# Performance work log

Hardware: AMD Instinct MI355X
Metric: run time of the kernel (lower is better)

## Reference

```python
import jax, jax.numpy as jnp
import numpy as np

D_MODEL = 1024
N_HEADS = 16


def setup_inputs() -> dict:
    key = jax.random.key(0)
    ks = jax.random.split(key, 11)
    B, S = 4, 2048
    sc = 1.0 / np.sqrt(D_MODEL)
    inp = {
        "Q": jax.random.normal(ks[0], (B, S, D_MODEL), jnp.float32),
        "K": jax.random.normal(ks[1], (B, S, D_MODEL), jnp.float32),
        "V": jax.random.normal(ks[2], (B, S, D_MODEL), jnp.float32),
        "Wq": jax.random.normal(ks[3], (D_MODEL, D_MODEL), jnp.float32) * sc,
        "bq": jnp.zeros((D_MODEL,), jnp.float32),
        "Wk": jax.random.normal(ks[4], (D_MODEL, D_MODEL), jnp.float32) * sc,
        "bk": jnp.zeros((D_MODEL,), jnp.float32),
        "Wv": jax.random.normal(ks[5], (D_MODEL, D_MODEL), jnp.float32) * sc,
        "bv": jnp.zeros((D_MODEL,), jnp.float32),
        "Wo": jax.random.normal(ks[6], (D_MODEL, D_MODEL), jnp.float32) * sc,
        "bo": jnp.zeros((D_MODEL,), jnp.float32),
    }
    return inp


def reference(Q, K, V, Wq, bq, Wk, bk, Wv, bv, Wo, bo):
    B, Sq, d_model = Q.shape
    h = N_HEADS
    d_k = d_model // h

    def split_heads(x, W, b):
        y = x @ W.T + b                     # (B, S, d_model)
        return y.reshape(B, x.shape[1], h, d_k).transpose(0, 2, 1, 3)  # (B,h,S,d_k)

    q = split_heads(Q, Wq, bq)
    k = split_heads(K, Wk, bk)
    v = split_heads(V, Wv, bv)

    scores = jnp.einsum("bhqd,bhkd->bhqk", q, k) / jnp.sqrt(jnp.asarray(d_k, q.dtype))
    attn = jax.nn.softmax(scores.astype(jnp.float32), axis=-1).astype(q.dtype)
    out = jnp.einsum("bhqk,bhkd->bhqd", attn, v)  # (B,h,Sq,d_k)
    out = out.transpose(0, 2, 1, 3).reshape(B, Sq, d_model)
    return out @ Wo.T + bo
```

## Files before the change

kernel.cpp:

```cpp
#include <hip/hip_runtime.h>
#include <stdint.h>

#define DM    1024
#define NH    16
#define DKH   64
#define SEQ   2048
#define NB    4
#define MROWS (NB * SEQ)

typedef __attribute__((ext_vector_type(4))) float f32x4;
typedef __attribute__((ext_vector_type(8))) short s16x8;
typedef __attribute__((ext_vector_type(4))) unsigned short u16x4;
typedef __attribute__((ext_vector_type(8))) unsigned short u16x8;

__device__ __forceinline__ unsigned short f2bf(float f) {
  union { float f; uint32_t u; } v; v.f = f;
  uint32_t r = v.u + 0x7fffu + ((v.u >> 16) & 1u);
  return (unsigned short)(r >> 16);
}

__device__ __forceinline__ void gload16(const void* g, void* l) {
  __builtin_amdgcn_global_load_lds(
      (__attribute__((address_space(1))) void*)(uintptr_t)g,
      (__attribute__((address_space(3))) void*)(uint32_t)(uintptr_t)l,
      16, 0, 0);
}

__device__ __forceinline__ float exp2fast(float x) {
#if __has_builtin(__builtin_amdgcn_exp2f)
  return __builtin_amdgcn_exp2f(x);
#else
  return exp2f(x);
#endif
}

__device__ __forceinline__ unsigned int cvtpk(float a, float b) {
  unsigned int r;
  asm("v_cvt_pk_bf16_f32 %0, %1, %2" : "=v"(r) : "v"(a), "v"(b));
  return r;
}

__device__ __forceinline__ float bperm(float v, int srclane) {
  union { float f; int i; } u; u.f = v;
  u.i = __builtin_amdgcn_ds_bpermute(srclane << 2, u.i);
  return u.f;
}

__device__ __forceinline__ void cvt8(const float* in, unsigned short* out, int i) {
  const f32x4* p = (const f32x4*)(in + i);
  f32x4 a = p[0], b = p[1];
  u16x8 r;
#pragma unroll
  for (int j = 0; j < 4; ++j) { r[j] = f2bf(a[j]); r[4 + j] = f2bf(b[j]); }
  *(u16x8*)(out + i) = r;
}

__global__ __launch_bounds__(256) void cvt4_kernel(const float* __restrict__ a,
                                                   const float* __restrict__ b,
                                                   const float* __restrict__ c,
                                                   const float* __restrict__ d,
                                                   unsigned short* __restrict__ oa,
                                                   unsigned short* __restrict__ ob,
                                                   unsigned short* __restrict__ oc,
                                                   unsigned short* __restrict__ od) {
  const int seg = blockIdx.x >> 9;
  const int blk = blockIdx.x & 511;
  const float* in = (seg == 0) ? a : (seg == 1) ? b : (seg == 2) ? c : d;
  unsigned short* out = (seg == 0) ? oa : (seg == 1) ? ob : (seg == 2) ? oc : od;
  cvt8(in, out, (blk * 256 + threadIdx.x) * 8);
}

template <int MODE, int AFP32>
__global__ __launch_bounds__(256) void gemm_bt(const void* __restrict__ Ap,
                                               const unsigned short* __restrict__ Bw,
                                               const float* __restrict__ bias,
                                               void* __restrict__ out,
                                               float oscale) {
  __shared__ char smem[65536];

  int bid = (int)(blockIdx.y * 8 + blockIdx.x);
  bid = (bid & 7) * 64 + (bid >> 3);
  const int tcol = (bid & 7) * 128;
  const int trow = (bid >> 3) * 128;

  const int lane = threadIdx.x & 63;
  const int w    = threadIdx.x >> 6;
  const int wm = w >> 1, wn = w & 1;
  const int l15 = lane & 15, l4 = lane >> 4;

  const float* Af = (const float*)Ap;
  const unsigned short* Ah = (const unsigned short*)Ap;

  const int srow = w * 8 + (lane >> 3);
  const int sc   = ((lane & 7) ^ (lane >> 3)) * 8;
  const int ldst = (lane & 7) * 16;

  f32x4 acc[4][4] = {};
  f32x4 areg[4][2];

  auto aload = [&](int k0) {
#pragma unroll
    for (int i = 0; i < 4; ++i) {
      const float* p = Af + (size_t)(trow + i * 32 + srow) * DM + k0 + sc;
      areg[i][0] = *(const f32x4*)p;
      areg[i][1] = *(const f32x4*)(p + 4);
    }
  };
  auto awrite = [&](int buf) {
    char* As = smem + buf * 32768;
#pragma unroll
    for (int i = 0; i < 4; ++i) {
      union { unsigned int u[4]; s16x8 v; } pu;
      pu.u[0] = cvtpk(areg[i][0][0], areg[i][0][1]);
      pu.u[1] = cvtpk(areg[i][0][2], areg[i][0][3]);
      pu.u[2] = cvtpk(areg[i][1][0], areg[i][1][1]);
      pu.u[3] = cvtpk(areg[i][1][2], areg[i][1][3]);
      *(s16x8*)(As + (i * 32 + srow) * 128 + ldst) = pu.v;
    }
  };
  auto astage = [&](int buf, int k0) {
    char* As = smem + buf * 32768;
#pragma unroll
    for (int i = 0; i < 4; ++i)
      gload16(Ah + (size_t)(trow + i * 32 + srow) * DM + k0 + sc, As + i * 4096 + w * 1024);
  };
  auto bstage = [&](int buf, int k0) {
    char* Bs = smem + buf * 32768 + 16384;
#pragma unroll
    for (int i = 0; i < 4; ++i)
      gload16(Bw + (size_t)(tcol + i * 32 + srow) * DM + k0 + sc, Bs + i * 4096 + w * 1024);
  };
  auto compute = [&](int buf) {
    char* As = smem + buf * 32768;
    char* Bs = As + 16384;
#pragma unroll
    for (int ks = 0; ks < 2; ++ks) {
      s16x8 af[4], bf[4];
#pragma unroll
      for (int x = 0; x < 4; ++x) {
        const int ra = wm * 64 + x * 16 + l15;
        const int rb = wn * 64 + x * 16 + l15;
        const int kb = ks * 4 + l4;
        af[x] = *(const s16x8*)(As + ra * 128 + ((kb ^ (ra & 7)) << 4));
        bf[x] = *(const s16x8*)(Bs + rb * 128 + ((kb ^ (rb & 7)) << 4));
      }
#pragma unroll
      for (int mi = 0; mi < 4; ++mi)
#pragma unroll
        for (int ni = 0; ni < 4; ++ni)
          acc[mi][ni] = __builtin_amdgcn_mfma_f32_16x16x32_bf16(af[mi], bf[ni], acc[mi][ni], 0, 0, 0);
    }
  };

  if (AFP32) aload(0); else astage(0, 0);
  bstage(0, 0);
  if (AFP32) awrite(0);
  __syncthreads();
  int cur = 0;

  for (int k0 = 0; k0 < DM; k0 += 64) {
    const bool more = (k0 + 64 < DM);
    if (more) {
      if (AFP32) aload(k0 + 64); else astage(cur ^ 1, k0 + 64);
      bstage(cur ^ 1, k0 + 64);
    }
    compute(cur);
    if (more && AFP32) awrite(cur ^ 1);
    __syncthreads();
    cur ^= 1;
  }

#pragma unroll
  for (int ni = 0; ni < 4; ++ni) {
    const int n  = tcol + wn * 64 + ni * 16 + l15;
    const float bv = bias[n];
#pragma unroll
    for (int mi = 0; mi < 4; ++mi) {
      const int m0 = trow + wm * 64 + mi * 16 + l4 * 4;
      if (MODE == 2) {
        float* o = (float*)out;
#pragma unroll
        for (int j = 0; j < 4; ++j)
          o[(size_t)(m0 + j) * DM + n] = acc[mi][ni][j] + bv;
      } else if (MODE == 0) {
        unsigned short* o = (unsigned short*)out;
        const int bb = m0 >> 11, h = n >> 6, dk = n & 63;
#pragma unroll
        for (int j = 0; j < 4; ++j) {
          const int s = (m0 + j) & 2047;
          o[(((size_t)bb * NH + h) * SEQ + s) * DKH + dk] = f2bf((acc[mi][ni][j] + bv) * oscale);
        }
      } else {
        unsigned short* o = (unsigned short*)out;
        const int bb = m0 >> 11, h = n >> 6, dk = n & 63, s = m0 & 2047;
        const int u = s & 31;
        const int s2 = (s & ~31) | ((u & 12) << 1) | ((u & 16) >> 2);
        u16x4 pk;
#pragma unroll
        for (int j = 0; j < 4; ++j) pk[j] = f2bf(acc[mi][ni][j] + bv);
        *(u16x4*)(o + (((size_t)bb * NH + h) * DKH + dk) * SEQ + s2) = pk;
      }
    }
  }
}

__global__ __launch_bounds__(256, 2) void attn_kernel(const unsigned short* __restrict__ qh,
                                                      const unsigned short* __restrict__ kh,
                                                      const unsigned short* __restrict__ vth,
                                                      unsigned short* __restrict__ ao) {
  __shared__ char smem[32768];

  int bid = (int)blockIdx.x;
  bid = (bid & 7) * 64 + (bid >> 3);
  const int bh = bid >> 3;
  const int q0 = (bid & 7) * 256;

  const int lane = threadIdx.x & 63;
  const int w    = threadIdx.x >> 6;
  const int l15 = lane & 15, l4 = lane >> 4;

  const int qrow = q0 + w * 64;
  const unsigned short* qbase = qh + ((size_t)bh * SEQ + qrow) * DKH;

  s16x8 qf[4][2];
#pragma unroll
  for (int ni = 0; ni < 4; ++ni)
#pragma unroll
    for (int ks = 0; ks < 2; ++ks)
      qf[ni][ks] = *(const s16x8*)(qbase + (ni * 16 + l15) * DKH + ks * 32 + l4 * 8);

  int koff[2][4], voff[2][4];
#pragma unroll
  for (int ks = 0; ks < 2; ++ks)
#pragma unroll
    for (int mi = 0; mi < 4; ++mi) {
      const int r = mi * 16 + l15;
      koff[ks][mi] = r * 128 + (((ks * 4 + l4) ^ (r & 7)) << 4);
    }
#pragma unroll
  for (int m = 0; m < 2; ++m)
#pragma unroll
    for (int nd = 0; nd < 4; ++nd) {
      const int r = nd * 16 + l15;
      voff[m][nd] = r * 128 + (((m * 4 + l4) ^ (r & 7)) << 4);
    }

  f32x4 o[4][4] = {};
  f32x4 lsum[4] = {};

  s16x8 onesB = (s16x8)0;
  if (l15 == 0) {
#pragma unroll
    for (int j = 0; j < 8; ++j) onesB[j] = (short)0x3F80;
  }

  const unsigned short* kbase = kh  + (size_t)bh * SEQ * DKH;
  const unsigned short* vbase = vth + (size_t)bh * DKH * SEQ;

  auto stageK = [&](int buf, int kv0) {
    char* Ks = smem + buf * 8192;
#pragma unroll
    for (int i = 0; i < 2; ++i) {
      const int row = i * 32 + w * 8 + (lane >> 3);
      const int sc  = ((lane & 7) ^ (row & 7)) << 3;
      gload16(kbase + (size_t)(kv0 + row) * DKH + sc, Ks + i * 4096 + w * 1024);
    }
  };
  auto stageV = [&](int buf, int kv0) {
    char* Vs = smem + 16384 + buf * 8192;
#pragma unroll
    for (int i = 0; i < 2; ++i) {
      const int row = i * 32 + w * 8 + (lane >> 3);
      const int sc  = ((lane & 7) ^ (row & 7)) << 3;
      gload16(vbase + (size_t)row * SEQ + kv0 + sc, Vs + i * 4096 + w * 1024);
    }
  };

  f32x4 sa[4][4];

  auto qkt = [&](const char* Ks) {
#pragma unroll
    for (int mi = 0; mi < 4; ++mi)
#pragma unroll
      for (int ni = 0; ni < 4; ++ni) sa[mi][ni] = (f32x4)0.f;
    __builtin_amdgcn_s_setprio(1);
#pragma unroll
    for (int ks = 0; ks < 2; ++ks) {
      s16x8 kf[4];
#pragma unroll
      for (int mi = 0; mi < 4; ++mi) kf[mi] = *(const s16x8*)(Ks + koff[ks][mi]);
#pragma unroll
      for (int mi = 0; mi < 4; ++mi)
#pragma unroll
        for (int ni = 0; ni < 4; ++ni)
          sa[mi][ni] = __builtin_amdgcn_mfma_f32_16x16x32_bf16(kf[mi], qf[ni][ks], sa[mi][ni], 0, 0, 0);
    }
    __builtin_amdgcn_s_setprio(0);
  };

  auto smpv = [&](const char* Vs) {
#pragma unroll
    for (int mi = 0; mi < 4; ++mi)
#pragma unroll
      for (int ni = 0; ni < 4; ++ni)
#pragma unroll
        for (int j = 0; j < 4; ++j)
          sa[mi][ni][j] = exp2fast(sa[mi][ni][j]);

    __builtin_amdgcn_s_setprio(1);
#pragma unroll
    for (int m = 0; m < 2; ++m) {
      s16x8 pa[4];
#pragma unroll
      for (int ni = 0; ni < 4; ++ni) {
        union { unsigned int u[4]; s16x8 v; } pu;
        pu.u[0] = cvtpk(sa[2 * m][ni][0],     sa[2 * m][ni][1]);
        pu.u[1] = cvtpk(sa[2 * m][ni][2],     sa[2 * m][ni][3]);
        pu.u[2] = cvtpk(sa[2 * m + 1][ni][0], sa[2 * m + 1][ni][1]);
        pu.u[3] = cvtpk(sa[2 * m + 1][ni][2], sa[2 * m + 1][ni][3]);
        pa[ni] = pu.v;
      }
#pragma unroll
      for (int ni = 0; ni < 4; ++ni)
        lsum[ni] = __builtin_amdgcn_mfma_f32_16x16x32_bf16(pa[ni], onesB, lsum[ni], 0, 0, 0);
#pragma unroll
      for (int nd = 0; nd < 4; ++nd) {
        const s16x8 vbf = *(const s16x8*)(Vs + voff[m][nd]);
#pragma unroll
        for (int ni = 0; ni < 4; ++ni)
          o[ni][nd] = __builtin_amdgcn_mfma_f32_16x16x32_bf16(pa[ni], vbf, o[ni][nd], 0, 0, 0);
      }
    }
    __builtin_amdgcn_s_setprio(0);
  };

  stageK(0, 0); stageV(0, 0);
  __syncthreads();

  for (int t = 0; t < 32; t += 2) {
    const int kv0 = t * 64;
    stageK(1, kv0 + 64); stageV(1, kv0 + 64);
    qkt(smem);
    smpv(smem + 16384);
    __syncthreads();
    if (t + 2 < 32) { stageK(0, kv0 + 128); stageV(0, kv0 + 128); }
    qkt(smem + 8192);
    smpv(smem + 16384 + 8192);
    __syncthreads();
  }

  const int bb = bh >> 4, h = bh & 15;
#pragma unroll
  for (int ni = 0; ni < 4; ++ni) {
#pragma unroll
    for (int j = 0; j < 4; ++j) {
      const float inv = 1.0f / bperm(lsum[ni][j], lane & 48);
      const int s = qrow + ni * 16 + l4 * 4 + j;
#pragma unroll
      for (int nd = 0; nd < 4; ++nd) {
        const int col = h * 64 + nd * 16 + l15;
        ao[((size_t)bb * SEQ + s) * DM + col] = f2bf(o[ni][nd][j] * inv);
      }
    }
  }
}

extern "C" void kernel_launch(void* const* d_in, const int* in_sizes, int n_in,
                              void* d_out, int out_size, void* d_ws, size_t ws_size,
                              hipStream_t stream) {
  const float* Q  = (const float*)d_in[0];
  const float* K  = (const float*)d_in[1];
  const float* V  = (const float*)d_in[2];
  const float* Wq = (const float*)d_in[3];
  const float* bq = (const float*)d_in[4];
  const float* Wk = (const float*)d_in[5];
  const float* bk = (const float*)d_in[6];
  const float* Wv = (const float*)d_in[7];
  const float* bv = (const float*)d_in[8];
  const float* Wo = (const float*)d_in[9];
  const float* bo = (const float*)d_in[10];
  float* out = (float*)d_out;

  char* ws = (char*)d_ws;
  const size_t MB = 1024 * 1024;
  unsigned short* Wqb = (unsigned short*)(ws + 0 * MB);
  unsigned short* Wkb = (unsigned short*)(ws + 2 * MB);
  unsigned short* Wvb = (unsigned short*)(ws + 4 * MB);
  unsigned short* Wob = (unsigned short*)(ws + 6 * MB);
  unsigned short* qhd = (unsigned short*)(ws + 8 * MB);
  unsigned short* khd = (unsigned short*)(ws + 24 * MB);
  unsigned short* vtd = (unsigned short*)(ws + 40 * MB);
  unsigned short* aod = (unsigned short*)(ws + 56 * MB);

  const float QSCALE = 0.18033688011112042f;

  cvt4_kernel<<<dim3(4 * 512), 256, 0, stream>>>(Wq, Wk, Wv, Wo, Wqb, Wkb, Wvb, Wob);

  dim3 gg(DM / 128, MROWS / 128);
  gemm_bt<0, 1><<<gg, 256, 0, stream>>>(Q, Wqb, bq, qhd, QSCALE);
  gemm_bt<0, 1><<<gg, 256, 0, stream>>>(K, Wkb, bk, khd, 1.0f);
  gemm_bt<1, 1><<<gg, 256, 0, stream>>>(V, Wvb, bv, vtd, 1.0f);

  attn_kernel<<<dim3(512), 256, 0, stream>>>(qhd, khd, vtd, aod);

  gemm_bt<2, 0><<<gg, 256, 0, stream>>>(aod, Wob, bo, out, 1.0f);
}
```

Baseline: 164.4 us.

## Merge QKV projections into one launch and use fine-grained waitcnt barriers

The three QKV projection GEMMs become a single launch, with blockIdx.z choosing the input, weight and output layout. This removes two launch gaps and gives more blocks in flight at once. In the GEMMs and the attention loop, full __syncthreads is replaced by explicit vmcnt/lgkmcnt waits plus s_barrier, so the next tile's loads can stay in flight while the current tile computes, and setprio is raised around the MFMA sections. The cost is that correctness now rests on hand-counted outstanding-load numbers. Also, the gemm_out loop drops the barrier after the last iteration and relies on the counts being right.

```diff
diff --git a/kernel.cpp b/kernel.cpp
--- a/kernel.cpp
+++ b/kernel.cpp
@@ -45,6 +45,11 @@
   u.i = __builtin_amdgcn_ds_bpermute(srclane << 2, u.i);
   return u.f;
 }
+
+#define WAIT_VM(N)  do { asm volatile("s_waitcnt vmcnt(" #N ")" ::: "memory"); \
+                         __builtin_amdgcn_sched_barrier(0); } while (0)
+#define WAIT_LGKM0  do { asm volatile("s_waitcnt lgkmcnt(0)" ::: "memory"); \
+                         __builtin_amdgcn_sched_barrier(0); } while (0)
 
 __device__ __forceinline__ void cvt8(const float* in, unsigned short* out, int i) {
   const f32x4* p = (const f32x4*)(in + i);
@@ -70,13 +75,28 @@
   cvt8(in, out, (blk * 256 + threadIdx.x) * 8);
 }
 
-template <int MODE, int AFP32>
-__global__ __launch_bounds__(256) void gemm_bt(const void* __restrict__ Ap,
-                                               const unsigned short* __restrict__ Bw,
-                                               const float* __restrict__ bias,
-                                               void* __restrict__ out,
-                                               float oscale) {
+__global__ __launch_bounds__(256) void gemm_qkv(const float* __restrict__ Aq,
+                                                const float* __restrict__ Ak,
+                                                const float* __restrict__ Av,
+                                                const unsigned short* __restrict__ Wq,
+                                                const unsigned short* __restrict__ Wk,
+                                                const unsigned short* __restrict__ Wv,
+                                                const float* __restrict__ biq,
+                                                const float* __restrict__ bik,
+                                                const float* __restrict__ biv,
+                                                unsigned short* __restrict__ oq,
+                                                unsigned short* __restrict__ ok,
+                                                unsigned short* __restrict__ ov,
+                                                float qscale) {
   __shared__ char smem[65536];
+
+  const int z = blockIdx.z;
+  const float* Af = (z == 0) ? Aq : (z == 1) ? Ak : Av;
+  const unsigned short* Bw = (z == 0) ? Wq : (z == 1) ? Wk : Wv;
+  const float* bias = (z == 0) ? biq : (z == 1) ? bik : biv;
+  unsigned short* out = (z == 0) ? oq : (z == 1) ? ok : ov;
+  const float oscale = (z == 0) ? qscale : 1.0f;
+  const int mode = (z == 2) ? 1 : 0;
 
   int bid = (int)(blockIdx.y * 8 + blockIdx.x);
   bid = (bid & 7) * 64 + (bid >> 3);
@@ -87,9 +107,6 @@
   const int w    = threadIdx.x >> 6;
   const int wm = w >> 1, wn = w & 1;
   const int l15 = lane & 15, l4 = lane >> 4;
-
-  const float* Af = (const float*)Ap;
-  const unsigned short* Ah = (const unsigned short*)Ap;
 
   const int srow = w * 8 + (lane >> 3);
   const int sc   = ((lane & 7) ^ (lane >> 3)) * 8;
@@ -118,12 +135,6 @@
       *(s16x8*)(As + (i * 32 + srow) * 128 + ldst) = pu.v;
     }
   };
-  auto astage = [&](int buf, int k0) {
-    char* As = smem + buf * 32768;
-#pragma unroll
-    for (int i = 0; i < 4; ++i)
-      gload16(Ah + (size_t)(trow + i * 32 + srow) * DM + k0 + sc, As + i * 4096 + w * 1024);
-  };
   auto bstage = [&](int buf, int k0) {
     char* Bs = smem + buf * 32768 + 16384;
 #pragma unroll
@@ -133,6 +144,7 @@
   auto compute = [&](int buf) {
     char* As = smem + buf * 32768;
     char* Bs = As + 16384;
+    __builtin_amdgcn_s_setprio(1);
 #pragma unroll
     for (int ks = 0; ks < 2; ++ks) {
       s16x8 af[4], bf[4];
@@ -150,23 +162,32 @@
         for (int ni = 0; ni < 4; ++ni)
           acc[mi][ni] = __builtin_amdgcn_mfma_f32_16x16x32_bf16(af[mi], bf[ni], acc[mi][ni], 0, 0, 0);
     }
-  };
-
-  if (AFP32) aload(0); else astage(0, 0);
+    __builtin_amdgcn_s_setprio(0);
+  };
+
+  aload(0);
   bstage(0, 0);
-  if (AFP32) awrite(0);
-  __syncthreads();
+  awrite(0);
+  WAIT_VM(0);
+  WAIT_LGKM0;
+  __builtin_amdgcn_s_barrier();
   int cur = 0;
 
   for (int k0 = 0; k0 < DM; k0 += 64) {
     const bool more = (k0 + 64 < DM);
     if (more) {
-      if (AFP32) aload(k0 + 64); else astage(cur ^ 1, k0 + 64);
+      aload(k0 + 64);
       bstage(cur ^ 1, k0 + 64);
+      WAIT_VM(12);
+    } else {
+      WAIT_VM(0);
     }
     compute(cur);
-    if (more && AFP32) awrite(cur ^ 1);
-    __syncthreads();
+    if (more) {
+      awrite(cur ^ 1);
+      WAIT_LGKM0;
+      __builtin_amdgcn_s_barrier();
+    }
     cur ^= 1;
   }
 
@@ -177,29 +198,108 @@
 #pragma unroll
     for (int mi = 0; mi < 4; ++mi) {
       const int m0 = trow + wm * 64 + mi * 16 + l4 * 4;
-      if (MODE == 2) {
-        float* o = (float*)out;
-#pragma unroll
-        for (int j = 0; j < 4; ++j)
-          o[(size_t)(m0 + j) * DM + n] = acc[mi][ni][j] + bv;
-      } else if (MODE == 0) {
-        unsigned short* o = (unsigned short*)out;
-        const int bb = m0 >> 11, h = n >> 6, dk = n & 63;
+      const int bb = m0 >> 11, h = n >> 6, dk = n & 63;
+      if (mode == 0) {
 #pragma unroll
         for (int j = 0; j < 4; ++j) {
           const int s = (m0 + j) & 2047;
-          o[(((size_t)bb * NH + h) * SEQ + s) * DKH + dk] = f2bf((acc[mi][ni][j] + bv) * oscale);
+          out[(((size_t)bb * NH + h) * SEQ + s) * DKH + dk] = f2bf((acc[mi][ni][j] + bv) * oscale);
         }
       } else {
-        unsigned short* o = (unsigned short*)out;
-        const int bb = m0 >> 11, h = n >> 6, dk = n & 63, s = m0 & 2047;
+        const int s = m0 & 2047;
         const int u = s & 31;
         const int s2 = (s & ~31) | ((u & 12) << 1) | ((u & 16) >> 2);
         u16x4 pk;
 #pragma unroll
         for (int j = 0; j < 4; ++j) pk[j] = f2bf(acc[mi][ni][j] + bv);
-        *(u16x4*)(o + (((size_t)bb * NH + h) * DKH + dk) * SEQ + s2) = pk;
+        *(u16x4*)(out + (((size_t)bb * NH + h) * DKH + dk) * SEQ + s2) = pk;
       }
+    }
+  }
+}
+
+__global__ __launch_bounds__(256) void gemm_out(const unsigned short* __restrict__ Ah,
+                                                const unsigned short* __restrict__ Bw,
+                                                const float* __restrict__ bias,
+                                                float* __restrict__ out) {
+  __shared__ char smem[65536];
+
+  int bid = (int)(blockIdx.y * 8 + blockIdx.x);
+  bid = (bid & 7) * 64 + (bid >> 3);
+  const int tcol = (bid & 7) * 128;
+  const int trow = (bid >> 3) * 128;
+
+  const int lane = threadIdx.x & 63;
+  const int w    = threadIdx.x >> 6;
+  const int wm = w >> 1, wn = w & 1;
+  const int l15 = lane & 15, l4 = lane >> 4;
+
+  const int srow = w * 8 + (lane >> 3);
+  const int sc   = ((lane & 7) ^ (lane >> 3)) * 8;
+
+  f32x4 acc[4][4] = {};
+
+  auto stage = [&](int buf, int k0) {
+    char* As = smem + buf * 32768;
+    char* Bs = As + 16384;
+#pragma unroll
+    for (int i = 0; i < 4; ++i) {
+      gload16(Ah + (size_t)(trow + i * 32 + srow) * DM + k0 + sc, As + i * 4096 + w * 1024);
+      gload16(Bw + (size_t)(tcol + i * 32 + srow) * DM + k0 + sc, Bs + i * 4096 + w * 1024);
+    }
+  };
+  auto compute = [&](int buf) {
+    char* As = smem + buf * 32768;
+    char* Bs = As + 16384;
+    __builtin_amdgcn_s_setprio(1);
+#pragma unroll
+    for (int ks = 0; ks < 2; ++ks) {
+      s16x8 af[4], bf[4];
+#pragma unroll
+      for (int x = 0; x < 4; ++x) {
+        const int ra = wm * 64 + x * 16 + l15;
+        const int rb = wn * 64 + x * 16 + l15;
+        const int kb = ks * 4 + l4;
+        af[x] = *(const s16x8*)(As + ra * 128 + ((kb ^ (ra & 7)) << 4));
+        bf[x] = *(const s16x8*)(Bs + rb * 128 + ((kb ^ (rb & 7)) << 4));
+      }
+#pragma unroll
+      for (int mi = 0; mi < 4; ++mi)
+#pragma unroll
+        for (int ni = 0; ni < 4; ++ni)
+          acc[mi][ni] = __builtin_amdgcn_mfma_f32_16x16x32_bf16(af[mi], bf[ni], acc[mi][ni], 0, 0, 0);
+    }
+    __builtin_amdgcn_s_setprio(0);
+  };
+
+  stage(0, 0);
+  WAIT_VM(0);
+  __builtin_amdgcn_s_barrier();
+  int cur = 0;
+
+  for (int k0 = 0; k0 < DM; k0 += 64) {
+    const bool more = (k0 + 64 < DM);
+    if (more) {
+      stage(cur ^ 1, k0 + 64);
+      WAIT_VM(8);
+    } else {
+      WAIT_VM(0);
+    }
+    compute(cur);
+    if (more) __builtin_amdgcn_s_barrier();
+    cur ^= 1;
+  }
+
+#pragma unroll
+  for (int ni = 0; ni < 4; ++ni) {
+    const int n  = tcol + wn * 64 + ni * 16 + l15;
+    const float bv = bias[n];
+#pragma unroll
+    for (int mi = 0; mi < 4; ++mi) {
+      const int m0 = trow + wm * 64 + mi * 16 + l4 * 4;
+#pragma unroll
+      for (int j = 0; j < 4; ++j)
+        out[(size_t)(m0 + j) * DM + n] = acc[mi][ni][j] + bv;
     }
   }
 }
@@ -257,22 +357,15 @@
   const unsigned short* kbase = kh  + (size_t)bh * SEQ * DKH;
   const unsigned short* vbase = vth + (size_t)bh * DKH * SEQ;
 
-  auto stageK = [&](int buf, int kv0) {
+  auto stageKV = [&](int buf, int kv0) {
     char* Ks = smem + buf * 8192;
+    char* Vs = smem + 16384 + buf * 8192;
 #pragma unroll
     for (int i = 0; i < 2; ++i) {
       const int row = i * 32 + w * 8 + (lane >> 3);
       const int sc  = ((lane & 7) ^ (row & 7)) << 3;
       gload16(kbase + (size_t)(kv0 + row) * DKH + sc, Ks + i * 4096 + w * 1024);
-    }
-  };
-  auto stageV = [&](int buf, int kv0) {
-    char* Vs = smem + 16384 + buf * 8192;
-#pragma unroll
-    for (int i = 0; i < 2; ++i) {
-      const int row = i * 32 + w * 8 + (lane >> 3);
-      const int sc  = ((lane & 7) ^ (row & 7)) << 3;
-      gload16(vbase + (size_t)row * SEQ + kv0 + sc, Vs + i * 4096 + w * 1024);
+      gload16(vbase + (size_t)row * SEQ + kv0 + sc,   Vs + i * 4096 + w * 1024);
     }
   };
 
@@ -334,19 +427,25 @@
     __builtin_amdgcn_s_setprio(0);
   };
 
-  stageK(0, 0); stageV(0, 0);
+  stageKV(0, 0);
   __syncthreads();
 
   for (int t = 0; t < 32; t += 2) {
     const int kv0 = t * 64;
-    stageK(1, kv0 + 64); stageV(1, kv0 + 64);
+    stageKV(1, kv0 + 64);
+    WAIT_VM(4);
     qkt(smem);
     smpv(smem + 16384);
-    __syncthreads();
-    if (t + 2 < 32) { stageK(0, kv0 + 128); stageV(0, kv0 + 128); }
+    __builtin_amdgcn_s_barrier();
+    if (t + 2 < 32) {
+      stageKV(0, kv0 + 128);
+      WAIT_VM(4);
+    } else {
+      WAIT_VM(0);
+    }
     qkt(smem + 8192);
     smpv(smem + 16384 + 8192);
-    __syncthreads();
+    __builtin_amdgcn_s_barrier();
   }
 
   const int bb = bh >> 4, h = bh & 15;
@@ -396,12 +495,11 @@
 
   cvt4_kernel<<<dim3(4 * 512), 256, 0, stream>>>(Wq, Wk, Wv, Wo, Wqb, Wkb, Wvb, Wob);
 
-  dim3 gg(DM / 128, MROWS / 128);
-  gemm_bt<0, 1><<<gg, 256, 0, stream>>>(Q, Wqb, bq, qhd, QSCALE);
-  gemm_bt<0, 1><<<gg, 256, 0, stream>>>(K, Wkb, bk, khd, 1.0f);
-  gemm_bt<1, 1><<<gg, 256, 0, stream>>>(V, Wvb, bv, vtd, 1.0f);
+  dim3 gg(DM / 128, MROWS / 128, 3);
+  gemm_qkv<<<gg, 256, 0, stream>>>(Q, K, V, Wqb, Wkb, Wvb, bq, bk, bv,
+                                   qhd, khd, vtd, QSCALE);
 
   attn_kernel<<<dim3(512), 256, 0, stream>>>(qhd, khd, vtd, aod);
 
-  gemm_bt<2, 0><<<gg, 256, 0, stream>>>(aod, Wob, bo, out, 1.0f);
-}
+  gemm_out<<<dim3(DM / 128, MROWS / 128), 256, 0, stream>>>(aod, Wob, bo, out);
+}
```

Result: slower. 174.6 us (+6.2%).
